# Optimization experiments

Measured on AMD Instinct MI355X. Metric: run time of the kernel, lower is better.

Reference implementation:

```python
import jax, jax.numpy as jnp
import numpy as np

NUM_EXPERTS = 64
TOP_K = 2


def setup_inputs() -> dict:
    key = jax.random.key(0)
    k1, k2 = jax.random.split(key)
    x = jax.random.normal(k1, (16384, 4096), dtype=jnp.float32)
    router_logits = jax.random.normal(k2, (16384, NUM_EXPERTS), dtype=jnp.float32)
    return {"x": x, "router_logits": router_logits}


def reference(x, router_logits):
    # router probs over experts
    router_probs = jax.nn.softmax(router_logits, axis=-1)            # [B, E]
    top_k_probs, top_k_indices = jax.lax.top_k(router_probs, TOP_K)  # [B, K]
    # renormalize selected probs
    top_k_probs = top_k_probs / jnp.sum(top_k_probs, axis=-1, keepdims=True)
    batch, dim = x.shape
    # token expansion: [B, D] -> [B*K, D]
    expanded_x = jnp.broadcast_to(x[:, None, :], (batch, TOP_K, dim)).reshape(-1, dim)
    expert_indices = top_k_indices.reshape(-1)   # [B*K] int32
    expert_weights = top_k_probs.reshape(-1)     # [B*K]
    return expanded_x, expert_indices, expert_weights
```

## Files before the change

### kernel.cpp

```cpp
#include <hip/hip_runtime.h>
#include <math.h>

#define NUM_EXPERTS 64
#define TOP_K 2

typedef float f32x4 __attribute__((ext_vector_type(4)));

__global__ void moe_fused_kernel(const f32x4* __restrict__ x4,
                                 f32x4* __restrict__ out4,
                                 int total4, int d4mask, int d4,
                                 const float* __restrict__ logits,
                                 float* __restrict__ idx_out,
                                 float* __restrict__ w_out,
                                 int batch, int rtrBlocks) {
    if ((int)blockIdx.x < rtrBlocks) {
        int lane   = threadIdx.x & 63;
        int wid    = (int)(blockIdx.x * blockDim.x + threadIdx.x) >> 6;
        int nWaves = (rtrBlocks * (int)blockDim.x) >> 6;
        for (int row = wid; row < batch; row += nWaves) {
            double l = (double)logits[row * NUM_EXPERTS + lane];

            double m = l;
            for (int off = 32; off; off >>= 1) {
                double o = __shfl_xor(m, off);
                m = (o > m) ? o : m;
            }
            double e = exp(l - m);
            double z = e;
            for (int off = 32; off; off >>= 1) z += __shfl_xor(z, off);
            double p = e / z;

            double v1 = p; int i1 = lane;
            for (int off = 1; off < 64; off <<= 1) {
                double ov = __shfl_xor(v1, off);
                int    oi = __shfl_xor(i1, off);
                if (ov > v1 || (ov == v1 && oi < i1)) { v1 = ov; i1 = oi; }
            }
            double v2 = (lane == i1) ? -1.0 : p; int i2 = lane;
            for (int off = 1; off < 64; off <<= 1) {
                double ov = __shfl_xor(v2, off);
                int    oi = __shfl_xor(i2, off);
                if (ov > v2 || (ov == v2 && oi < i2)) { v2 = ov; i2 = oi; }
            }

            if (lane == 0) {
                double s = v1 + v2;
                idx_out[2 * row]     = (float)i1;
                idx_out[2 * row + 1] = (float)i2;
                w_out[2 * row]       = (float)(v1 / s);
                w_out[2 * row + 1]   = (float)(v2 / s);
            }
        }
        return;
    }

    int ebid   = (int)blockIdx.x - rtrBlocks;
    int stride = ((int)gridDim.x - rtrBlocks) * (int)blockDim.x;
    int i      = ebid * (int)blockDim.x + (int)threadIdx.x;

    for (; i + 3 * stride < total4; i += 4 * stride) {
        int ia = i, ib = i + stride, ic = i + 2 * stride, id = i + 3 * stride;
        f32x4 v0 = x4[ia];
        f32x4 v1 = x4[ib];
        f32x4 v2 = x4[ic];
        f32x4 v3 = x4[id];
        int d0 = 2 * ia - (ia & d4mask);
        int d1 = 2 * ib - (ib & d4mask);
        int d2 = 2 * ic - (ic & d4mask);
        int d3 = 2 * id - (id & d4mask);
        __builtin_nontemporal_store(v0, &out4[d0]);
        __builtin_nontemporal_store(v0, &out4[d0 + d4]);
        __builtin_nontemporal_store(v1, &out4[d1]);
        __builtin_nontemporal_store(v1, &out4[d1 + d4]);
        __builtin_nontemporal_store(v2, &out4[d2]);
        __builtin_nontemporal_store(v2, &out4[d2 + d4]);
        __builtin_nontemporal_store(v3, &out4[d3]);
        __builtin_nontemporal_store(v3, &out4[d3 + d4]);
    }
    for (; i < total4; i += stride) {
        f32x4 v = x4[i];
        int dst = 2 * i - (i & d4mask);
        __builtin_nontemporal_store(v, &out4[dst]);
        __builtin_nontemporal_store(v, &out4[dst + d4]);
    }
}

extern "C" void kernel_launch(void* const* d_in, const int* in_sizes, int n_in,
                              void* d_out, int out_size, void* d_ws, size_t ws_size,
                              hipStream_t stream) {
    const float* x      = (const float*)d_in[0];
    const float* logits = (const float*)d_in[1];
    float* out = (float*)d_out;

    const int batch = in_sizes[1] / NUM_EXPERTS;
    const int dim   = in_sizes[0] / batch;
    const int d4    = dim / 4;

    const long long exp_elems = (long long)batch * TOP_K * dim;
    float* idx_out = out + exp_elems;
    float* w_out   = idx_out + (long long)batch * TOP_K;

    const int total4    = batch * d4;
    const int rtrBlocks = 256;
    const int expBlocks = 2048;
    moe_fused_kernel<<<rtrBlocks + expBlocks, 256, 0, stream>>>(
        (const f32x4*)x, (f32x4*)out, total4, d4 - 1, d4,
        logits, idx_out, w_out, batch, rtrBlocks);
}
```

Before: 147.9 us.

## Assign contiguous chunks per expansion block and unroll copy loop to eight loads

```diff
diff --git a/kernel.cpp b/kernel.cpp
--- a/kernel.cpp
+++ b/kernel.cpp
@@ -54,30 +54,30 @@
         return;
     }
 
-    int ebid   = (int)blockIdx.x - rtrBlocks;
-    int stride = ((int)gridDim.x - rtrBlocks) * (int)blockDim.x;
-    int i      = ebid * (int)blockDim.x + (int)threadIdx.x;
+    int ebid    = (int)blockIdx.x - rtrBlocks;
+    int nexp    = (int)gridDim.x - rtrBlocks;
+    int chunk   = (total4 + nexp - 1) / nexp;
+    int begin   = ebid * chunk;
+    int end     = begin + chunk; if (end > total4) end = total4;
+    int bstride = (int)blockDim.x;
 
-    for (; i + 3 * stride < total4; i += 4 * stride) {
-        int ia = i, ib = i + stride, ic = i + 2 * stride, id = i + 3 * stride;
-        f32x4 v0 = x4[ia];
-        f32x4 v1 = x4[ib];
-        f32x4 v2 = x4[ic];
-        f32x4 v3 = x4[id];
-        int d0 = 2 * ia - (ia & d4mask);
-        int d1 = 2 * ib - (ib & d4mask);
-        int d2 = 2 * ic - (ic & d4mask);
-        int d3 = 2 * id - (id & d4mask);
-        __builtin_nontemporal_store(v0, &out4[d0]);
-        __builtin_nontemporal_store(v0, &out4[d0 + d4]);
-        __builtin_nontemporal_store(v1, &out4[d1]);
-        __builtin_nontemporal_store(v1, &out4[d1 + d4]);
-        __builtin_nontemporal_store(v2, &out4[d2]);
-        __builtin_nontemporal_store(v2, &out4[d2 + d4]);
-        __builtin_nontemporal_store(v3, &out4[d3]);
-        __builtin_nontemporal_store(v3, &out4[d3 + d4]);
+    int i = begin + (int)threadIdx.x;
+    for (; i + 7 * bstride < end; i += 8 * bstride) {
+        f32x4 v[8];
+        int   d[8];
+#pragma unroll
+        for (int k = 0; k < 8; ++k) {
+            int ii = i + k * bstride;
+            v[k] = x4[ii];
+            d[k] = 2 * ii - (ii & d4mask);
+        }
+#pragma unroll
+        for (int k = 0; k < 8; ++k) {
+            __builtin_nontemporal_store(v[k], &out4[d[k]]);
+            __builtin_nontemporal_store(v[k], &out4[d[k] + d4]);
+        }
     }
-    for (; i < total4; i += stride) {
+    for (; i < end; i += bstride) {
         f32x4 v = x4[i];
         int dst = 2 * i - (i & d4mask);
         __builtin_nontemporal_store(v, &out4[dst]);
```

Measured after the change: 123.9 us. -16.2%, faster.
